# Performance work log

Measured on AMD Instinct MI355X. Metric: run time of the kernel, lower is better.

The kernel has to match this reference:

```python
import jax, jax.numpy as jnp
import numpy as np

B, IN, H = 4096, 1024, 2048


def setup_inputs() -> dict:
    key = jax.random.key(0)
    ks = jax.random.split(key, 7)
    return {
        "x": jax.random.normal(ks[0], (B, IN), jnp.float32),
        "h": jax.random.normal(ks[1], (B, H), jnp.float32),
        "c": jax.random.normal(ks[2], (B, H), jnp.float32),
        "w_ih": jax.random.normal(ks[3], (4 * H, IN), jnp.float32) * 0.02,
        "w_hh": jax.random.normal(ks[4], (4 * H, H), jnp.float32) * 0.02,
        "b_ih": jax.random.normal(ks[5], (4 * H,), jnp.float32) * 0.02,
        "b_hh": jax.random.normal(ks[6], (4 * H,), jnp.float32) * 0.02,
    }


def reference(x, h, c, w_ih, w_hh, b_ih, b_hh):
    act = jnp.sin  # custom gate activation (Sine_activation repo)
    # Combined GEMMs: same math as the 8 separate F.linear calls.
    # gates: [B, 4H], chunk order along dim 0 of weights: f, i, ic, o
    gates = (x @ w_ih.T + b_ih) + (h @ w_hh.T + b_hh)
    f_in, i_in, ic_in, o_in = jnp.split(gates, 4, axis=-1)
    ft = jax.nn.sigmoid(f_in)
    it = jax.nn.sigmoid(i_in)
    i_cands = act(ic_in)
    ct = c * ft + i_cands * it
    ot = jax.nn.sigmoid(o_in)
    ht = ot * act(ct)
    return (ht, ct)
```

## Files before the change

### kernel.cpp

```cpp
#include <hip/hip_runtime.h>

typedef __attribute__((ext_vector_type(8))) short short8;
typedef __attribute__((ext_vector_type(4))) float f32x4;

#define BDIM 4096
#define INDIM 1024
#define HDIM 2048
#define KDIM 3072
#define NDIM 8192
#define OUT_HALF 8388608
#define NKT 96

__device__ __forceinline__ unsigned short f2bf(float f) {
  unsigned u = __float_as_uint(f);
  u += 0x7FFFu + ((u >> 16) & 1u);
  return (unsigned short)(u >> 16);
}

__device__ __forceinline__ float sigmoidf_(float x) {
  return 1.0f / (1.0f + __expf(-x));
}

__global__ __launch_bounds__(256) void pack_a(const float* __restrict__ x,
                                              const float* __restrict__ hh,
                                              unsigned short* __restrict__ A) {
  int idx = blockIdx.x * 256 + threadIdx.x;
  int m = idx / 384;
  int k0 = (idx - m * 384) * 8;
  const float* src = (k0 < INDIM) ? (x + (size_t)m * INDIM + k0)
                                  : (hh + (size_t)m * HDIM + (k0 - INDIM));
  float4 lo = ((const float4*)src)[0];
  float4 hi = ((const float4*)src)[1];
  union { unsigned short us[8]; uint4 v; } o;
  o.us[0] = f2bf(lo.x); o.us[1] = f2bf(lo.y); o.us[2] = f2bf(lo.z); o.us[3] = f2bf(lo.w);
  o.us[4] = f2bf(hi.x); o.us[5] = f2bf(hi.y); o.us[6] = f2bf(hi.z); o.us[7] = f2bf(hi.w);
  *(uint4*)(A + (size_t)m * KDIM + k0) = o.v;
}

__global__ __launch_bounds__(256) void pack_w(const float* __restrict__ w_ih,
                                              const float* __restrict__ w_hh,
                                              const float* __restrict__ b_ih,
                                              const float* __restrict__ b_hh,
                                              unsigned short* __restrict__ W,
                                              float* __restrict__ bias) {
  int idx = blockIdx.x * 256 + threadIdx.x;
  int np = idx / 384;
  int rem = idx - np * 384;
  int k0 = rem * 8;
  int j = np >> 2;
  int g = np & 3;
  int n = g * HDIM + j;
  const float* src = (k0 < INDIM) ? (w_ih + (size_t)n * INDIM + k0)
                                  : (w_hh + (size_t)n * HDIM + (k0 - INDIM));
  float4 lo = ((const float4*)src)[0];
  float4 hi = ((const float4*)src)[1];
  union { unsigned short us[8]; uint4 v; } o;
  o.us[0] = f2bf(lo.x); o.us[1] = f2bf(lo.y); o.us[2] = f2bf(lo.z); o.us[3] = f2bf(lo.w);
  o.us[4] = f2bf(hi.x); o.us[5] = f2bf(hi.y); o.us[6] = f2bf(hi.z); o.us[7] = f2bf(hi.w);
  *(uint4*)(W + (size_t)np * KDIM + k0) = o.v;
  if (rem == 0) bias[np] = b_ih[n] + b_hh[n];
}

__device__ __forceinline__ void gload_lds16(const void* g, void* l) {
  __builtin_amdgcn_global_load_lds(
      (const __attribute__((address_space(1))) void*)g,
      (__attribute__((address_space(3))) void*)l, 16, 0, 0);
}

#define SB0 __builtin_amdgcn_sched_barrier(0)

__global__ __launch_bounds__(512, 2) void lstm_gemm(
    const unsigned short* __restrict__ A,
    const unsigned short* __restrict__ W,
    const float* __restrict__ bias,
    const float* __restrict__ c,
    float* __restrict__ out) {
  extern __shared__ char smem[];

  const int tid = threadIdx.x;
  const int lane = tid & 63;
  const int wid = tid >> 6;

  const int bid = blockIdx.x;
  const int local = bid >> 3;
  const int tm = (bid & 7) * 2 + (local & 1);
  const int tn = local >> 1;

  int rowA0, clA0, rowA1, clA1;
  {
    int P0 = wid * 1024 + lane * 16;
    int P1 = 8192 + wid * 1024 + lane * 16;
    int r2, cp, cg;
    r2 = P0 >> 7; cp = (P0 >> 4) & 7; cg = cp ^ (r2 & 7);
    rowA0 = r2 * 2 + (cg >> 2); clA0 = cg & 3;
    r2 = P1 >> 7; cp = (P1 >> 4) & 7; cg = cp ^ (r2 & 7);
    rowA1 = r2 * 2 + (cg >> 2); clA1 = cg & 3;
  }
  const unsigned short* srcA0 = A + (size_t)(tm * 256 + rowA0) * KDIM + clA0 * 8;
  const unsigned short* srcA1 = A + (size_t)(tm * 256 + rowA1) * KDIM + clA1 * 8;
  const unsigned short* srcB0 = W + (size_t)(tn * 256 + rowA0) * KDIM + clA0 * 8;
  const unsigned short* srcB1 = W + (size_t)(tn * 256 + rowA1) * KDIM + clA1 * 8;
  const int ldA0 = wid * 1024;
  const int ldA1 = 8192 + wid * 1024;
  const int ldB0 = 16384 + wid * 1024;
  const int ldB1 = 24576 + wid * 1024;

  const int fr = lane & 15;
  const int fq = lane >> 4;
  const int wr = wid >> 2;
  const int wc = wid & 3;
  const int frh = fr >> 1;
  const int clA = (((fr & 1) << 2) | fq) ^ frh;
  const int aconst = wr * 8192 + frh * 128 + clA * 16;
  const int bconst = 16384 + wc * 4096 + frh * 128 + clA * 16;

  f32x4 acc[8][4] = {};
  short8 af[4], bf_[4], ag[4];

#pragma unroll
  for (int tt = 0; tt < 3; ++tt) {
    char* lb = smem + tt * 32768;
    gload_lds16(srcA0 + tt * 32, lb + ldA0);
    gload_lds16(srcA1 + tt * 32, lb + ldA1);
    gload_lds16(srcB0 + tt * 32, lb + ldB0);
    gload_lds16(srcB1 + tt * 32, lb + ldB1);
  }
  asm volatile("s_waitcnt vmcnt(8)" ::: "memory");
  __builtin_amdgcn_s_barrier(); SB0;
#pragma unroll
  for (int mi = 0; mi < 4; ++mi)
    af[mi] = *(const short8*)(smem + aconst + mi * 1024);
#pragma unroll
  for (int ni = 0; ni < 4; ++ni)
    bf_[ni] = *(const short8*)(smem + bconst + ni * 1024);

#define TILE_BODY(T, VMSTR, STAGE_, PREF_)                                   \
  do {                                                                       \
    const char* rb = smem + ((T) & 3) * 32768;                               \
    const char* rbn = smem + (((T) + 1) & 3) * 32768;                        \
    char* lb = smem + (((T) + 3) & 3) * 32768;                               \
    if (STAGE_) {                                                            \
      gload_lds16(srcA0 + (size_t)((T) + 3) * 32, lb + ldA0);                \
      gload_lds16(srcA1 + (size_t)((T) + 3) * 32, lb + ldA1);                \
    }                                                                        \
    _Pragma("unroll")                                                        \
    for (int mi = 0; mi < 4; ++mi)                                           \
      ag[mi] = *(const short8*)(rb + aconst + (mi + 4) * 1024);              \
    SB0;                                                                     \
    __builtin_amdgcn_s_setprio(1);                                           \
    _Pragma("unroll")                                                        \
    for (int mi = 0; mi < 4; ++mi)                                           \
      _Pragma("unroll")                                                      \
      for (int ni = 0; ni < 4; ++ni)                                         \
        acc[mi][ni] = __builtin_amdgcn_mfma_f32_16x16x32_bf16(               \
            af[mi], bf_[ni], acc[mi][ni], 0, 0, 0);                          \
    __builtin_amdgcn_s_setprio(0);                                           \
    if (STAGE_) {                                                            \
      gload_lds16(srcB0 + (size_t)((T) + 3) * 32, lb + ldB0);                \
      gload_lds16(srcB1 + (size_t)((T) + 3) * 32, lb + ldB1);                \
    }                                                                        \
    asm volatile("s_waitcnt vmcnt(" VMSTR ")" ::: "memory");                 \
    asm volatile("s_waitcnt lgkmcnt(0)" ::: "memory");                       \
    __builtin_amdgcn_s_barrier(); SB0;                                       \
    if (PREF_) {                                                             \
      _Pragma("unroll")                                                      \
      for (int mi = 0; mi < 4; ++mi)                                         \
        af[mi] = *(const short8*)(rbn + aconst + mi * 1024);                 \
    }                                                                        \
    SB0;                                                                     \
    __builtin_amdgcn_s_setprio(1);                                           \
    _Pragma("unroll")                                                        \
    for (int mi = 0; mi < 4; ++mi)                                           \
      _Pragma("unroll")                                                      \
      for (int ni = 0; ni < 4; ++ni)                                         \
        acc[mi + 4][ni] = __builtin_amdgcn_mfma_f32_16x16x32_bf16(           \
            ag[mi], bf_[ni], acc[mi + 4][ni], 0, 0, 0);                      \
    __builtin_amdgcn_s_setprio(0);                                           \
    if (PREF_) {                                                             \
      _Pragma("unroll")                                                      \
      for (int ni = 0; ni < 4; ++ni)                                         \
        bf_[ni] = *(const short8*)(rbn + bconst + ni * 1024);                \
    }                                                                        \
  } while (0)

  for (int t = 0; t < NKT - 3; ++t) TILE_BODY(t, "8", true, true);
  TILE_BODY(NKT - 3, "4", false, true);
  TILE_BODY(NKT - 2, "0", false, true);
  TILE_BODY(NKT - 1, "0", false, false);
#undef TILE_BODY

  const int jw = fr;
  const int jg = tn * 64 + wc * 16 + jw;
  const f32x4 bi = *(const f32x4*)(bias + tn * 256 + wc * 64 + jw * 4);
  float* ep = (float*)smem + wid * 1024;

#pragma unroll
  for (int mi = 0; mi < 8; ++mi) {
#pragma unroll
    for (int ni = 0; ni < 4; ++ni)
#pragma unroll
      for (int r = 0; r < 4; ++r)
        ep[(fq * 4 + r) * 64 + ni * 16 + fr] = acc[mi][ni][r];
    asm volatile("s_waitcnt lgkmcnt(0)" ::: "memory");
#pragma unroll
    for (int t4 = 0; t4 < 4; ++t4) {
      const int row = fq + t4 * 4;
      f32x4 g4 = *(const f32x4*)(ep + row * 64 + jw * 4);
      const float f_in = g4[0] + bi[0];
      const float i_in = g4[1] + bi[1];
      const float ic_in = g4[2] + bi[2];
      const float o_in = g4[3] + bi[3];
      const float ft = sigmoidf_(f_in);
      const float it = sigmoidf_(i_in);
      const float ics = __sinf(ic_in);
      const int mg = tm * 256 + wr * 128 + mi * 16 + row;
      const float cv = c[(size_t)mg * HDIM + jg];
      const float ct = cv * ft + ics * it;
      const float ot = sigmoidf_(o_in);
      const float ht = ot * __sinf(ct);
      out[(size_t)mg * HDIM + jg] = ht;
      out[OUT_HALF + (size_t)mg * HDIM + jg] = ct;
    }
    asm volatile("s_waitcnt lgkmcnt(0)" ::: "memory");
  }
}

extern "C" void kernel_launch(void* const* d_in, const int* in_sizes, int n_in,
                              void* d_out, int out_size, void* d_ws, size_t ws_size,
                              hipStream_t stream) {
  const float* x    = (const float*)d_in[0];
  const float* h    = (const float*)d_in[1];
  const float* c    = (const float*)d_in[2];
  const float* w_ih = (const float*)d_in[3];
  const float* w_hh = (const float*)d_in[4];
  const float* b_ih = (const float*)d_in[5];
  const float* b_hh = (const float*)d_in[6];
  float* out = (float*)d_out;

  char* ws = (char*)d_ws;
  unsigned short* Abf = (unsigned short*)ws;
  unsigned short* Wbf = (unsigned short*)(ws + 25165824);
  float* bias = (float*)(ws + 25165824 + 50331648);

  hipFuncSetAttribute((const void*)lstm_gemm,
                      hipFuncAttributeMaxDynamicSharedMemorySize, 131072);

  pack_a<<<6144, 256, 0, stream>>>(x, h, Abf);
  pack_w<<<12288, 256, 0, stream>>>(w_ih, w_hh, b_ih, b_hh, Wbf, bias);
  lstm_gemm<<<512, 512, 131072, stream>>>(Abf, Wbf, bias, c, out);
}
```

Baseline: 222.6 us.

## Merge pack kernels, double-buffer B fragments, pad epilogue LDS, incrementalize pointers

Fuses the two fp32-to-bf16 pack kernels into a single launch, which removes one kernel launch and the gap between them. In the GEMM main loop, B fragments now alternate between two register sets so the next tile's B loads are issued together with the A loads right after the barrier. This replaces the old trailing B prefetch that ran after the second MFMA block, and costs extra VGPRs. Global source pointers are advanced incrementally instead of recomputed per tile, and the two waitcnts are merged into one. The epilogue LDS row stride is padded from 64 to 68 floats to reduce bank conflicts.

```diff
diff --git a/kernel.cpp b/kernel.cpp
--- a/kernel.cpp
+++ b/kernel.cpp
@@ -10,6 +10,7 @@
 #define NDIM 8192
 #define OUT_HALF 8388608
 #define NKT 96
+#define ACHUNKS 1572864
 
 __device__ __forceinline__ unsigned short f2bf(float f) {
   unsigned u = __float_as_uint(f);
@@ -21,44 +22,42 @@
   return 1.0f / (1.0f + __expf(-x));
 }
 
-__global__ __launch_bounds__(256) void pack_a(const float* __restrict__ x,
-                                              const float* __restrict__ hh,
-                                              unsigned short* __restrict__ A) {
+__global__ __launch_bounds__(256) void pack_all(
+    const float* __restrict__ x, const float* __restrict__ hh,
+    const float* __restrict__ w_ih, const float* __restrict__ w_hh,
+    const float* __restrict__ b_ih, const float* __restrict__ b_hh,
+    unsigned short* __restrict__ A, unsigned short* __restrict__ W,
+    float* __restrict__ bias) {
   int idx = blockIdx.x * 256 + threadIdx.x;
-  int m = idx / 384;
-  int k0 = (idx - m * 384) * 8;
-  const float* src = (k0 < INDIM) ? (x + (size_t)m * INDIM + k0)
-                                  : (hh + (size_t)m * HDIM + (k0 - INDIM));
-  float4 lo = ((const float4*)src)[0];
-  float4 hi = ((const float4*)src)[1];
-  union { unsigned short us[8]; uint4 v; } o;
-  o.us[0] = f2bf(lo.x); o.us[1] = f2bf(lo.y); o.us[2] = f2bf(lo.z); o.us[3] = f2bf(lo.w);
-  o.us[4] = f2bf(hi.x); o.us[5] = f2bf(hi.y); o.us[6] = f2bf(hi.z); o.us[7] = f2bf(hi.w);
-  *(uint4*)(A + (size_t)m * KDIM + k0) = o.v;
-}
-
-__global__ __launch_bounds__(256) void pack_w(const float* __restrict__ w_ih,
-                                              const float* __restrict__ w_hh,
-                                              const float* __restrict__ b_ih,
-                                              const float* __restrict__ b_hh,
-                                              unsigned short* __restrict__ W,
-                                              float* __restrict__ bias) {
-  int idx = blockIdx.x * 256 + threadIdx.x;
-  int np = idx / 384;
-  int rem = idx - np * 384;
-  int k0 = rem * 8;
-  int j = np >> 2;
-  int g = np & 3;
-  int n = g * HDIM + j;
-  const float* src = (k0 < INDIM) ? (w_ih + (size_t)n * INDIM + k0)
-                                  : (w_hh + (size_t)n * HDIM + (k0 - INDIM));
-  float4 lo = ((const float4*)src)[0];
-  float4 hi = ((const float4*)src)[1];
-  union { unsigned short us[8]; uint4 v; } o;
-  o.us[0] = f2bf(lo.x); o.us[1] = f2bf(lo.y); o.us[2] = f2bf(lo.z); o.us[3] = f2bf(lo.w);
-  o.us[4] = f2bf(hi.x); o.us[5] = f2bf(hi.y); o.us[6] = f2bf(hi.z); o.us[7] = f2bf(hi.w);
-  *(uint4*)(W + (size_t)np * KDIM + k0) = o.v;
-  if (rem == 0) bias[np] = b_ih[n] + b_hh[n];
+  if (idx < ACHUNKS) {
+    int m = idx / 384;
+    int k0 = (idx - m * 384) * 8;
+    const float* src = (k0 < INDIM) ? (x + (size_t)m * INDIM + k0)
+                                    : (hh + (size_t)m * HDIM + (k0 - INDIM));
+    float4 lo = ((const float4*)src)[0];
+    float4 hi = ((const float4*)src)[1];
+    union { unsigned short us[8]; uint4 v; } o;
+    o.us[0] = f2bf(lo.x); o.us[1] = f2bf(lo.y); o.us[2] = f2bf(lo.z); o.us[3] = f2bf(lo.w);
+    o.us[4] = f2bf(hi.x); o.us[5] = f2bf(hi.y); o.us[6] = f2bf(hi.z); o.us[7] = f2bf(hi.w);
+    *(uint4*)(A + (size_t)m * KDIM + k0) = o.v;
+  } else {
+    idx -= ACHUNKS;
+    int np = idx / 384;
+    int rem = idx - np * 384;
+    int k0 = rem * 8;
+    int j = np >> 2;
+    int g = np & 3;
+    int n = g * HDIM + j;
+    const float* src = (k0 < INDIM) ? (w_ih + (size_t)n * INDIM + k0)
+                                    : (w_hh + (size_t)n * HDIM + (k0 - INDIM));
+    float4 lo = ((const float4*)src)[0];
+    float4 hi = ((const float4*)src)[1];
+    union { unsigned short us[8]; uint4 v; } o;
+    o.us[0] = f2bf(lo.x); o.us[1] = f2bf(lo.y); o.us[2] = f2bf(lo.z); o.us[3] = f2bf(lo.w);
+    o.us[4] = f2bf(hi.x); o.us[5] = f2bf(hi.y); o.us[6] = f2bf(hi.z); o.us[7] = f2bf(hi.w);
+    *(uint4*)(W + (size_t)np * KDIM + k0) = o.v;
+    if (rem == 0) bias[np] = b_ih[n] + b_hh[n];
+  }
 }
 
 __device__ __forceinline__ void gload_lds16(const void* g, void* l) {
@@ -96,10 +95,10 @@
     r2 = P1 >> 7; cp = (P1 >> 4) & 7; cg = cp ^ (r2 & 7);
     rowA1 = r2 * 2 + (cg >> 2); clA1 = cg & 3;
   }
-  const unsigned short* srcA0 = A + (size_t)(tm * 256 + rowA0) * KDIM + clA0 * 8;
-  const unsigned short* srcA1 = A + (size_t)(tm * 256 + rowA1) * KDIM + clA1 * 8;
-  const unsigned short* srcB0 = W + (size_t)(tn * 256 + rowA0) * KDIM + clA0 * 8;
-  const unsigned short* srcB1 = W + (size_t)(tn * 256 + rowA1) * KDIM + clA1 * 8;
+  const unsigned short* gA0 = A + (size_t)(tm * 256 + rowA0) * KDIM + clA0 * 8;
+  const unsigned short* gA1 = A + (size_t)(tm * 256 + rowA1) * KDIM + clA1 * 8;
+  const unsigned short* gB0 = W + (size_t)(tn * 256 + rowA0) * KDIM + clA0 * 8;
+  const unsigned short* gB1 = W + (size_t)(tn * 256 + rowA1) * KDIM + clA1 * 8;
   const int ldA0 = wid * 1024;
   const int ldA1 = 8192 + wid * 1024;
   const int ldB0 = 16384 + wid * 1024;
@@ -115,15 +114,16 @@
   const int bconst = 16384 + wc * 4096 + frh * 128 + clA * 16;
 
   f32x4 acc[8][4] = {};
-  short8 af[4], bf_[4], ag[4];
+  short8 af[4], ag[4], bfA[4], bfB[4];
 
 #pragma unroll
   for (int tt = 0; tt < 3; ++tt) {
     char* lb = smem + tt * 32768;
-    gload_lds16(srcA0 + tt * 32, lb + ldA0);
-    gload_lds16(srcA1 + tt * 32, lb + ldA1);
-    gload_lds16(srcB0 + tt * 32, lb + ldB0);
-    gload_lds16(srcB1 + tt * 32, lb + ldB1);
+    gload_lds16(gA0, lb + ldA0);
+    gload_lds16(gA1, lb + ldA1);
+    gload_lds16(gB0, lb + ldB0);
+    gload_lds16(gB1, lb + ldB1);
+    gA0 += 32; gA1 += 32; gB0 += 32; gB1 += 32;
   }
   asm volatile("s_waitcnt vmcnt(8)" ::: "memory");
   __builtin_amdgcn_s_barrier(); SB0;
@@ -132,16 +132,16 @@
     af[mi] = *(const short8*)(smem + aconst + mi * 1024);
 #pragma unroll
   for (int ni = 0; ni < 4; ++ni)
-    bf_[ni] = *(const short8*)(smem + bconst + ni * 1024);
-
-#define TILE_BODY(T, VMSTR, STAGE_, PREF_)                                   \
+    bfA[ni] = *(const short8*)(smem + bconst + ni * 1024);
+
+#define TILE_BODY(T, VMSTR, STAGE_, PREF_, BFC, BFN)                         \
   do {                                                                       \
     const char* rb = smem + ((T) & 3) * 32768;                               \
     const char* rbn = smem + (((T) + 1) & 3) * 32768;                        \
     char* lb = smem + (((T) + 3) & 3) * 32768;                               \
     if (STAGE_) {                                                            \
-      gload_lds16(srcA0 + (size_t)((T) + 3) * 32, lb + ldA0);                \
-      gload_lds16(srcA1 + (size_t)((T) + 3) * 32, lb + ldA1);                \
+      gload_lds16(gA0, lb + ldA0);                                           \
+      gload_lds16(gA1, lb + ldA1);                                           \
     }                                                                        \
     _Pragma("unroll")                                                        \
     for (int mi = 0; mi < 4; ++mi)                                           \
@@ -153,19 +153,23 @@
       _Pragma("unroll")                                                      \
       for (int ni = 0; ni < 4; ++ni)                                         \
         acc[mi][ni] = __builtin_amdgcn_mfma_f32_16x16x32_bf16(               \
-            af[mi], bf_[ni], acc[mi][ni], 0, 0, 0);                          \
+            af[mi], BFC[ni], acc[mi][ni], 0, 0, 0);                          \
     __builtin_amdgcn_s_setprio(0);                                           \
     if (STAGE_) {                                                            \
-      gload_lds16(srcB0 + (size_t)((T) + 3) * 32, lb + ldB0);                \
-      gload_lds16(srcB1 + (size_t)((T) + 3) * 32, lb + ldB1);                \
+      gload_lds16(gB0, lb + ldB0);                                           \
+      gload_lds16(gB1, lb + ldB1);                                           \
+      gA0 += 32; gA1 += 32; gB0 += 32; gB1 += 32;                            \
     }                                                                        \
-    asm volatile("s_waitcnt vmcnt(" VMSTR ")" ::: "memory");                 \
-    asm volatile("s_waitcnt lgkmcnt(0)" ::: "memory");                       \
+    asm volatile("s_waitcnt vmcnt(" VMSTR ") lgkmcnt(0)" ::: "memory");      \
+    SB0;                                                                     \
     __builtin_amdgcn_s_barrier(); SB0;                                       \
     if (PREF_) {                                                             \
       _Pragma("unroll")                                                      \
       for (int mi = 0; mi < 4; ++mi)                                         \
         af[mi] = *(const short8*)(rbn + aconst + mi * 1024);                 \
+      _Pragma("unroll")                                                      \
+      for (int ni = 0; ni < 4; ++ni)                                         \
+        BFN[ni] = *(const short8*)(rbn + bconst + ni * 1024);                \
     }                                                                        \
     SB0;                                                                     \
     __builtin_amdgcn_s_setprio(1);                                           \
@@ -174,25 +178,24 @@
       _Pragma("unroll")                                                      \
       for (int ni = 0; ni < 4; ++ni)                                         \
         acc[mi + 4][ni] = __builtin_amdgcn_mfma_f32_16x16x32_bf16(           \
-            ag[mi], bf_[ni], acc[mi + 4][ni], 0, 0, 0);                      \
+            ag[mi], BFC[ni], acc[mi + 4][ni], 0, 0, 0);                      \
     __builtin_amdgcn_s_setprio(0);                                           \
-    if (PREF_) {                                                             \
-      _Pragma("unroll")                                                      \
-      for (int ni = 0; ni < 4; ++ni)                                         \
-        bf_[ni] = *(const short8*)(rbn + bconst + ni * 1024);                \
-    }                                                                        \
   } while (0)
 
-  for (int t = 0; t < NKT - 3; ++t) TILE_BODY(t, "8", true, true);
-  TILE_BODY(NKT - 3, "4", false, true);
-  TILE_BODY(NKT - 2, "0", false, true);
-  TILE_BODY(NKT - 1, "0", false, false);
+  for (int t = 0; t < 92; t += 2) {
+    TILE_BODY(t,     "8", true, true, bfA, bfB);
+    TILE_BODY(t + 1, "8", true, true, bfB, bfA);
+  }
+  TILE_BODY(92, "8", true,  true,  bfA, bfB);
+  TILE_BODY(93, "4", false, true,  bfB, bfA);
+  TILE_BODY(94, "0", false, true,  bfA, bfB);
+  TILE_BODY(95, "0", false, false, bfB, bfA);
 #undef TILE_BODY
 
   const int jw = fr;
   const int jg = tn * 64 + wc * 16 + jw;
   const f32x4 bi = *(const f32x4*)(bias + tn * 256 + wc * 64 + jw * 4);
-  float* ep = (float*)smem + wid * 1024;
+  float* ep = (float*)smem + wid * 1152;
 
 #pragma unroll
   for (int mi = 0; mi < 8; ++mi) {
@@ -200,12 +203,12 @@
     for (int ni = 0; ni < 4; ++ni)
 #pragma unroll
       for (int r = 0; r < 4; ++r)
-        ep[(fq * 4 + r) * 64 + ni * 16 + fr] = acc[mi][ni][r];
+        ep[(fq * 4 + r) * 68 + ni * 16 + fr] = acc[mi][ni][r];
     asm volatile("s_waitcnt lgkmcnt(0)" ::: "memory");
 #pragma unroll
     for (int t4 = 0; t4 < 4; ++t4) {
       const int row = fq + t4 * 4;
-      f32x4 g4 = *(const f32x4*)(ep + row * 64 + jw * 4);
+      f32x4 g4 = *(const f32x4*)(ep + row * 68 + jw * 4);
       const float f_in = g4[0] + bi[0];
       const float i_in = g4[1] + bi[1];
       const float ic_in = g4[2] + bi[2];
@@ -245,7 +248,6 @@
   hipFuncSetAttribute((const void*)lstm_gemm,
                       hipFuncAttributeMaxDynamicSharedMemorySize, 131072);
 
-  pack_a<<<6144, 256, 0, stream>>>(x, h, Abf);
-  pack_w<<<12288, 256, 0, stream>>>(w_ih, w_hh, b_ih, b_hh, Wbf, bias);
+  pack_all<<<18432, 256, 0, stream>>>(x, h, w_ih, w_hh, b_ih, b_hh, Abf, Wbf, bias);
   lstm_gemm<<<512, 512, 131072, stream>>>(Abf, Wbf, bias, c, out);
 }
```

Result: no change. 223.0 us (+0.2%).
